# Optimization experiments

Measured on AMD Instinct MI355X. Metric: run time of the kernel, lower is better.

## Reference

```python
import jax, jax.numpy as jnp
import numpy as np

BITS = 4
MASK = (1 << BITS) - 1  # 15


def _dequant(qweight, scales, qzeros, groupsize):
    # qweight: [in//32*bits, out] int32; 8 nibbles packed per int32 along rows.
    out_f = qweight.shape[1]
    shifts = jnp.arange(0, 32, BITS, dtype=jnp.int32)  # [8]
    # [rows, 8, out] -> unpacked int weights in [0, 15]
    w = (qweight[:, None, :] >> shifts[None, :, None]) & MASK
    w = w.reshape(-1, groupsize, out_f)  # [n_groups, groupsize, out]
    s = scales.reshape(-1, 1, out_f)     # [n_groups, 1, out]
    z = qzeros.reshape(-1, 1, out_f)
    W = s * w.astype(scales.dtype) - z * s
    return W.reshape(-1, out_f)          # [in, out]


def setup_inputs() -> dict:
    key = jax.random.key(0)
    k1, k2, k3, k4, k5 = jax.random.split(key, 5)
    B, S, IN, OUT, G = 4, 2048, 4096, 4096, 64
    x = jax.random.normal(k1, (B, S, IN), dtype=jnp.float16)
    qweight = jax.random.randint(k2, (IN // 32 * BITS, OUT), 0, 2147483647, dtype=jnp.int32)
    scales = (jax.random.uniform(k3, (IN // G, OUT), dtype=jnp.float32) * 0.01 + 0.001).astype(jnp.float16)
    qzeros = (jax.random.uniform(k4, (IN // G, OUT), dtype=jnp.float32) * 15.0).astype(jnp.float16)
    bias = jax.random.normal(k5, (OUT,), dtype=jnp.float16)
    return {"x": x, "qweight": qweight, "scales": scales, "qzeros": qzeros,
            "bias": bias, "groupsize": G, "bits": BITS}


def reference(x, qweight, scales, qzeros, bias, groupsize, bits):
    W = _dequant(qweight, scales, qzeros, groupsize)  # [in, out] fp16
    return jnp.matmul(x, W) + bias
```

## Files before the change

kernel.cpp:

```cpp
#include <hip/hip_runtime.h>
#include <stdint.h>
#include <stddef.h>

typedef __bf16 bf16;
typedef __bf16 bf16x8 __attribute__((ext_vector_type(8)));
typedef float  f32x4  __attribute__((ext_vector_type(4)));

#define GLOBAL_AS(p) ((const __attribute__((address_space(1))) void*)(p))
#define LDS_AS(p)    ((__attribute__((address_space(3))) void*)(p))

__device__ __forceinline__ void gload_lds16(const bf16* g, bf16* l) {
    __builtin_amdgcn_global_load_lds(GLOBAL_AS(g), LDS_AS(l), 16, 0, 0);
}

__global__ __launch_bounds__(256)
void convert_x_kernel(const float* __restrict__ x, bf16* __restrict__ xb, long n8) {
    long t = (long)blockIdx.x * blockDim.x + threadIdx.x;
    if (t >= n8) return;
    const f32x4* p = (const f32x4*)(x + t * 8);
    f32x4 a = p[0], b = p[1];
    bf16x8 v;
#pragma unroll
    for (int j = 0; j < 4; ++j) { v[j] = (bf16)a[j]; v[4 + j] = (bf16)b[j]; }
    *(bf16x8*)(xb + t * 8) = v;
}

__global__ __launch_bounds__(256)
void dequant_wt64_kernel(const uint32_t* __restrict__ qw,
                         const float* __restrict__ scales,
                         const float* __restrict__ qzeros,
                         bf16* __restrict__ Wt,
                         int N, int K, int rows_per_group) {
    const int i = blockIdx.x * 256 + threadIdx.x;
    const int w = i >> 6, l = i & 63;
    const int nr8 = K >> 6;
    const int r8 = w % nr8;
    const int o  = (w / nr8) * 8 + (l >> 3);
    const int rr = l & 7;
    const int r  = r8 * 8 + rr;
    if (o >= N) return;
    const uint32_t q = qw[(size_t)r * N + o];
    const int g = r / rows_per_group;
    const float s = scales[(size_t)g * N + o];
    const float z = qzeros[(size_t)g * N + o];
    const float nsz = -s * z;
    bf16x8 v;
#pragma unroll
    for (int j = 0; j < 8; ++j)
        v[j] = (bf16)fmaf((float)((q >> (4 * j)) & 15u), s, nsz);
    *(bf16x8*)(Wt + ((size_t)r8 * N + o) * 64 + rr * 8) = v;
}

constexpr int BM2 = 256, BN2 = 256, BK2 = 64;

#define SB()    __builtin_amdgcn_sched_barrier(0)
#define BAR()   __builtin_amdgcn_s_barrier()
#define LGKM0() asm volatile("s_waitcnt lgkmcnt(0)" ::: "memory")
#define VMCNT(N) asm volatile("s_waitcnt vmcnt(" #N ")" ::: "memory")

#define MFMA_HALF(A, B, IBASE)                                             \
    _Pragma("unroll")                                                      \
    for (int i_ = 0; i_ < 4; ++i_) {                                       \
        _Pragma("unroll")                                                  \
        for (int j_ = 0; j_ < 4; ++j_)                                     \
            acc[(IBASE) + i_][j_] = __builtin_amdgcn_mfma_f32_16x16x32_bf16( \
                (A)[(IBASE) + i_], (B)[j_], acc[(IBASE) + i_][j_], 0, 0, 0); \
    }

#define PHASE_TAIL(A, B, IBASE)                          \
    SB();                                                \
    __builtin_amdgcn_s_setprio(1);                       \
    MFMA_HALF(A, B, IBASE);                              \
    __builtin_amdgcn_s_setprio(0);                       \
    LGKM0();                                             \
    BAR();                                               \
    SB()

#define PHASE_TAIL_VM4(A, B, IBASE)                      \
    SB();                                                \
    __builtin_amdgcn_s_setprio(1);                       \
    MFMA_HALF(A, B, IBASE);                              \
    __builtin_amdgcn_s_setprio(0);                       \
    LGKM0();                                             \
    VMCNT(4);                                            \
    BAR();                                               \
    SB()

#define READ_A4(DST, BUF, KH, LO)                                          \
    _Pragma("unroll")                                                      \
    for (int i_ = (LO); i_ < (LO) + 4; ++i_)                               \
        DST[i_] = *(const bf16x8*)(&As[BUF][(wm * 128 + i_ * 16 + lrow) * 64 \
                                           + (((lhi + 4 * (KH)) ^ swz) * 8)]);
#define READ_B4(DST, BUF, KH)                                              \
    _Pragma("unroll")                                                      \
    for (int j_ = 0; j_ < 4; ++j_)                                         \
        DST[j_] = *(const bf16x8*)(&Bs[BUF][(wn * 64 + j_ * 16 + lrow) * 64 \
                                           + (((lhi + 4 * (KH)) ^ swz) * 8)]);

__global__ __launch_bounds__(512, 2)
void gemm8_kernel(const bf16* __restrict__ Ab,
                  const bf16* __restrict__ Bt,
                  const float* __restrict__ bias,
                  float* __restrict__ out,
                  int M, int N, int K, int nbx) {
    __shared__ __align__(16) bf16 As[2][BM2 * BK2];
    __shared__ __align__(16) bf16 Bs[2][BN2 * BK2];

    const int tid  = threadIdx.x;
    const int lane = tid & 63;
    const int wave = tid >> 6;
    const int wm = wave >> 2;
    const int wn = wave & 3;

    const int nwg = gridDim.x;
    int wg = blockIdx.x;
    {
        const int q = nwg >> 3, r = nwg & 7;
        const int xcd = wg & 7, off = wg >> 3;
        wg = (xcd < r ? xcd * (q + 1) : r * (q + 1) + (xcd - r) * q) + off;
    }
    const int nby = nwg / nbx;
    const int bx = wg / nby;
    const int by = wg % nby;
    const int m0 = by * BM2;
    const int n0 = bx * BN2;

    const int lrow = lane & 15;
    const int lhi  = lane >> 4;
    const int swz  = (lrow >> 1) & 7;

    const int NT = K >> 6;
    const int NI = NT >> 1;

    const bf16* aSrc[2][2];
    const bf16* bSrc[2][2];
#pragma unroll
    for (int h = 0; h < 2; ++h)
#pragma unroll
        for (int it = 0; it < 2; ++it) {
            const int q  = tid + it * 512;
            const int rl = q >> 3;
            const int cl = (q & 7) ^ ((rl >> 1) & 7);
            aSrc[h][it] = Ab + (size_t)(m0 + h * 128 + rl) * K + cl * 8;
            bSrc[h][it] = Bt + (size_t)(n0 + h * 128 + rl) * 64 + cl * 8;
        }
    const size_t aStride = 64;
    const size_t bStride = (size_t)N * 64;

    auto stageA = [&](int tIdx, int buf) {
#pragma unroll
        for (int h = 0; h < 2; ++h)
#pragma unroll
            for (int it = 0; it < 2; ++it) {
                const int q = tid + it * 512;
                gload_lds16(aSrc[h][it] + (size_t)tIdx * aStride,
                            &As[buf][h * 8192 + q * 8]);
            }
    };
    auto stageB = [&](int tIdx, int buf) {
#pragma unroll
        for (int h = 0; h < 2; ++h)
#pragma unroll
            for (int it = 0; it < 2; ++it) {
                const int q = tid + it * 512;
                gload_lds16(bSrc[h][it] + (size_t)tIdx * bStride,
                            &Bs[buf][h * 8192 + q * 8]);
            }
    };

    f32x4 acc[8][4];
#pragma unroll
    for (int i = 0; i < 8; ++i)
#pragma unroll
        for (int j = 0; j < 4; ++j) acc[i][j] = (f32x4){0.f, 0.f, 0.f, 0.f};

    stageA(0, 0); stageB(0, 0); stageA(1, 1);
    VMCNT(4);
    BAR();
    SB();

    bf16x8 fa0[8], fa1[8], fb0[4], fb1[4];
    READ_A4(fa0, 0, 0, 0);
    READ_B4(fb0, 0, 0);

    for (int i2 = 0; i2 < NI; ++i2) {
        const int t0  = 2 * i2;
        const int tB1 = t0 + 1;
        const int tS2 = (t0 + 2 < NT) ? t0 + 2 : NT - 1;
        const int tS3 = (t0 + 3 < NT) ? t0 + 3 : NT - 1;

        READ_A4(fa0, 0, 0, 4);
        READ_B4(fb1, 0, 1);
        stageB(tB1, 1);
        PHASE_TAIL(fa0, fb0, 0);

        READ_A4(fa1, 0, 1, 0);
        PHASE_TAIL(fa0, fb0, 4);

        READ_A4(fa1, 0, 1, 4);
        stageB(tS2, 0);
        PHASE_TAIL_VM4(fa1, fb1, 0);

        READ_A4(fa0, 1, 0, 0);
        READ_B4(fb0, 1, 0);
        stageA(tS2, 0);
        PHASE_TAIL(fa1, fb1, 4);

        READ_A4(fa0, 1, 0, 4);
        READ_B4(fb1, 1, 1);
        PHASE_TAIL(fa0, fb0, 0);

        READ_A4(fa1, 1, 1, 0);
        READ_A4(fa1, 1, 1, 4);
        PHASE_TAIL(fa0, fb0, 4);

        stageA(tS3, 1);
        PHASE_TAIL_VM4(fa1, fb1, 0);

        READ_A4(fa0, 0, 0, 0);
        READ_B4(fb0, 0, 0);
        PHASE_TAIL(fa1, fb1, 4);
    }

    asm volatile("s_waitcnt vmcnt(0)" ::: "memory");

#pragma unroll
    for (int j = 0; j < 4; ++j) {
        const int col = n0 + wn * 64 + j * 16 + lrow;
        const float bv = bias[col];
#pragma unroll
        for (int i = 0; i < 8; ++i) {
            const int rbase = m0 + wm * 128 + i * 16 + lhi * 4;
#pragma unroll
            for (int r = 0; r < 4; ++r)
                out[(size_t)(rbase + r) * N + col] = acc[i][j][r] + bv;
        }
    }
}

constexpr int BM = 128, BN = 128, BK = 32;

__global__ __launch_bounds__(256)
void gemm_fused_kernel(const float* __restrict__ Af,
                       const uint32_t* __restrict__ qw,
                       const float* __restrict__ scales,
                       const float* __restrict__ qzeros,
                       const float* __restrict__ bias,
                       float* __restrict__ out,
                       int M, int N, int K, int G) {
    __shared__ __align__(16) bf16 As2[BM * BK];
    __shared__ __align__(16) bf16 Bs2[BN * BK];

    const int tid  = threadIdx.x;
    const int lane = tid & 63;
    const int wave = tid >> 6;
    const int wmm = wave & 1;
    const int wnn = wave >> 1;
    const int m0 = blockIdx.y * BM;
    const int n0 = blockIdx.x * BN;

    const int lr = lane & 15;
    const int lk8 = (lane >> 4) * 8;

    f32x4 acc[4][4];
#pragma unroll
    for (int i = 0; i < 4; ++i)
#pragma unroll
        for (int j = 0; j < 4; ++j) acc[i][j] = (f32x4){0.f, 0.f, 0.f, 0.f};

    for (int kt = 0; kt < K; kt += BK) {
#pragma unroll
        for (int it = 0; it < 2; ++it) {
            const int c = tid + it * 256;
            const int row = c >> 2;
            const int kc  = (c & 3) * 8;
            const f32x4* p = (const f32x4*)(Af + (size_t)(m0 + row) * K + kt + kc);
            f32x4 a = p[0], b = p[1];
            bf16x8 v;
#pragma unroll
            for (int j = 0; j < 4; ++j) { v[j] = (bf16)a[j]; v[4 + j] = (bf16)b[j]; }
            *(bf16x8*)(As2 + row * BK + kc) = v;
        }
        const int g = kt / G;
#pragma unroll
        for (int it = 0; it < 2; ++it) {
            const int idx = tid + it * 256;
            const int rl = idx >> 7;
            const int nl = idx & 127;
            uint32_t q = qw[(size_t)(kt / 8 + rl) * N + n0 + nl];
            float s = scales[(size_t)g * N + n0 + nl];
            float z = qzeros[(size_t)g * N + n0 + nl];
            float nsz = -s * z;
            bf16x8 v;
#pragma unroll
            for (int j = 0; j < 8; ++j)
                v[j] = (bf16)fmaf((float)((q >> (4 * j)) & 15u), s, nsz);
            *(bf16x8*)(Bs2 + nl * BK + rl * 8) = v;
        }
        __syncthreads();

        bf16x8 a[4], b[4];
#pragma unroll
        for (int i = 0; i < 4; ++i)
            a[i] = *(const bf16x8*)(As2 + (wmm * 64 + i * 16 + lr) * BK + lk8);
#pragma unroll
        for (int j = 0; j < 4; ++j)
            b[j] = *(const bf16x8*)(Bs2 + (wnn * 64 + j * 16 + lr) * BK + lk8);

#pragma unroll
        for (int i = 0; i < 4; ++i)
#pragma unroll
            for (int j = 0; j < 4; ++j)
                acc[i][j] = __builtin_amdgcn_mfma_f32_16x16x32_bf16(
                    a[i], b[j], acc[i][j], 0, 0, 0);
        __syncthreads();
    }

#pragma unroll
    for (int j = 0; j < 4; ++j) {
        const int col = n0 + wnn * 64 + j * 16 + (lane & 15);
        const float bv = bias[col];
#pragma unroll
        for (int i = 0; i < 4; ++i) {
            const int rbase = m0 + wmm * 64 + i * 16 + (lane >> 4) * 4;
#pragma unroll
            for (int r = 0; r < 4; ++r)
                out[(size_t)(rbase + r) * N + col] = acc[i][j][r] + bv;
        }
    }
}

extern "C" void kernel_launch(void* const* d_in, const int* in_sizes, int n_in,
                              void* d_out, int out_size, void* d_ws, size_t ws_size,
                              hipStream_t stream) {
    const float*    x      = (const float*)d_in[0];
    const uint32_t* qw     = (const uint32_t*)d_in[1];
    const float*    scales = (const float*)d_in[2];
    const float*    qzeros = (const float*)d_in[3];
    const float*    bias   = (const float*)d_in[4];
    float*          out    = (float*)d_out;

    const int N = in_sizes[4];
    const int K = (in_sizes[1] / N) * 8;
    const int M = in_sizes[0] / K;
    const int G = K / (in_sizes[2] / N);

    const size_t xb_bytes = (size_t)M * K * sizeof(bf16);
    const size_t wt_bytes = (size_t)N * K * sizeof(bf16);

    const bool shape_ok = (M % BM2 == 0) && (N % BN2 == 0) && (K % 128 == 0) &&
                          (G % 8 == 0);

    if (shape_ok && ws_size >= xb_bytes + wt_bytes) {
        bf16* Xb = (bf16*)d_ws;
        bf16* Wt = (bf16*)((char*)d_ws + xb_bytes);
        const long n8 = (long)M * K / 8;
        convert_x_kernel<<<(int)((n8 + 255) / 256), 256, 0, stream>>>(x, Xb, n8);
        const long dq_threads = ((long)K >> 6) * (N / 8) * 64;
        dequant_wt64_kernel<<<(int)((dq_threads + 255) / 256), 256, 0, stream>>>(
            qw, scales, qzeros, Wt, N, K, G / 8);
        const int nbx = N / BN2;
        const int nwg = nbx * (M / BM2);
        gemm8_kernel<<<nwg, 512, 0, stream>>>(Xb, Wt, bias, out, M, N, K, nbx);
    } else {
        dim3 grid(N / BN, M / BM);
        gemm_fused_kernel<<<grid, 256, 0, stream>>>(
            x, qw, scales, qzeros, bias, out, M, N, K, G);
    }
}
```

Measured before the change: 518.2 us.

## Restructure GEMM main loop with half-tile staging and relaxed LDS waits

Splits the A/B global-to-LDS staging into per-half loads interleaved across the eight MFMA phases, and reorders which operand is prefetched (B ahead by one tile instead of A). Most phases drop the full lgkmcnt(0) wait and barrier-per-phase in favor of partial lgkmcnt(8) waits and fewer waits, so LDS reads overlap more with MFMAs. This aims to spread memory traffic evenly and cut stall time at barriers, but risks race hazards if the looser waits let reads see buffers still being overwritten.

```diff
diff --git a/kernel.cpp b/kernel.cpp
--- a/kernel.cpp
+++ b/kernel.cpp
@@ -55,8 +55,10 @@
 
 #define SB()    __builtin_amdgcn_sched_barrier(0)
 #define BAR()   __builtin_amdgcn_s_barrier()
-#define LGKM0() asm volatile("s_waitcnt lgkmcnt(0)" ::: "memory")
+#define LGKM(N) asm volatile("s_waitcnt lgkmcnt(" #N ")" ::: "memory")
 #define VMCNT(N) asm volatile("s_waitcnt vmcnt(" #N ")" ::: "memory")
+#define PRIO1() __builtin_amdgcn_s_setprio(1)
+#define PRIO0() __builtin_amdgcn_s_setprio(0)
 
 #define MFMA_HALF(A, B, IBASE)                                             \
     _Pragma("unroll")                                                      \
@@ -66,25 +68,6 @@
             acc[(IBASE) + i_][j_] = __builtin_amdgcn_mfma_f32_16x16x32_bf16( \
                 (A)[(IBASE) + i_], (B)[j_], acc[(IBASE) + i_][j_], 0, 0, 0); \
     }
-
-#define PHASE_TAIL(A, B, IBASE)                          \
-    SB();                                                \
-    __builtin_amdgcn_s_setprio(1);                       \
-    MFMA_HALF(A, B, IBASE);                              \
-    __builtin_amdgcn_s_setprio(0);                       \
-    LGKM0();                                             \
-    BAR();                                               \
-    SB()
-
-#define PHASE_TAIL_VM4(A, B, IBASE)                      \
-    SB();                                                \
-    __builtin_amdgcn_s_setprio(1);                       \
-    MFMA_HALF(A, B, IBASE);                              \
-    __builtin_amdgcn_s_setprio(0);                       \
-    LGKM0();                                             \
-    VMCNT(4);                                            \
-    BAR();                                               \
-    SB()
 
 #define READ_A4(DST, BUF, KH, LO)                                          \
     _Pragma("unroll")                                                      \
@@ -147,25 +130,21 @@
     const size_t aStride = 64;
     const size_t bStride = (size_t)N * 64;
 
-    auto stageA = [&](int tIdx, int buf) {
-#pragma unroll
-        for (int h = 0; h < 2; ++h)
-#pragma unroll
-            for (int it = 0; it < 2; ++it) {
-                const int q = tid + it * 512;
-                gload_lds16(aSrc[h][it] + (size_t)tIdx * aStride,
-                            &As[buf][h * 8192 + q * 8]);
-            }
+    auto stageAh = [&](int tIdx, int half, int buf) {
+#pragma unroll
+        for (int it = 0; it < 2; ++it) {
+            const int q = tid + it * 512;
+            gload_lds16(aSrc[half][it] + (size_t)tIdx * aStride,
+                        &As[buf][half * 8192 + q * 8]);
+        }
     };
-    auto stageB = [&](int tIdx, int buf) {
-#pragma unroll
-        for (int h = 0; h < 2; ++h)
-#pragma unroll
-            for (int it = 0; it < 2; ++it) {
-                const int q = tid + it * 512;
-                gload_lds16(bSrc[h][it] + (size_t)tIdx * bStride,
-                            &Bs[buf][h * 8192 + q * 8]);
-            }
+    auto stageBh = [&](int tIdx, int half, int buf) {
+#pragma unroll
+        for (int it = 0; it < 2; ++it) {
+            const int q = tid + it * 512;
+            gload_lds16(bSrc[half][it] + (size_t)tIdx * bStride,
+                        &Bs[buf][half * 8192 + q * 8]);
+        }
     };
 
     f32x4 acc[8][4];
@@ -174,52 +153,79 @@
 #pragma unroll
         for (int j = 0; j < 4; ++j) acc[i][j] = (f32x4){0.f, 0.f, 0.f, 0.f};
 
-    stageA(0, 0); stageB(0, 0); stageA(1, 1);
+    stageAh(0, 0, 0); stageAh(0, 1, 0); stageBh(0, 0, 0); stageBh(0, 1, 0);
+    stageBh(1, 0, 1); stageBh(1, 1, 1);
     VMCNT(4);
     BAR();
     SB();
 
     bf16x8 fa0[8], fa1[8], fb0[4], fb1[4];
-    READ_A4(fa0, 0, 0, 0);
-    READ_B4(fb0, 0, 0);
 
     for (int i2 = 0; i2 < NI; ++i2) {
-        const int t0  = 2 * i2;
-        const int tB1 = t0 + 1;
-        const int tS2 = (t0 + 2 < NT) ? t0 + 2 : NT - 1;
-        const int tS3 = (t0 + 3 < NT) ? t0 + 3 : NT - 1;
-
+        const int tE  = 2 * i2;
+        const int tO  = tE + 1;
+        const int tE2 = (tE + 2 < NT) ? tE + 2 : NT - 1;
+        const int tO2 = (tE + 3 < NT) ? tE + 3 : NT - 1;
+
+        READ_A4(fa0, 0, 0, 0);
+        READ_B4(fb0, 0, 0);
         READ_A4(fa0, 0, 0, 4);
+        stageAh(tO, 0, 1);
+        SB();
+        PRIO1(); MFMA_HALF(fa0, fb0, 0); PRIO0();
+        BAR(); SB();
+
         READ_B4(fb1, 0, 1);
-        stageB(tB1, 1);
-        PHASE_TAIL(fa0, fb0, 0);
-
+        SB();
         READ_A4(fa1, 0, 1, 0);
-        PHASE_TAIL(fa0, fb0, 4);
-
         READ_A4(fa1, 0, 1, 4);
-        stageB(tS2, 0);
-        PHASE_TAIL_VM4(fa1, fb1, 0);
+        stageAh(tO, 1, 1);
+        SB();
+        PRIO1(); MFMA_HALF(fa0, fb0, 4); PRIO0();
+        LGKM(8); SB();
+        BAR(); SB();
+
+        stageBh(tE2, 0, 0);
+        SB();
+        PRIO1(); MFMA_HALF(fa1, fb1, 0); PRIO0();
+        BAR(); SB();
+
+        stageBh(tE2, 1, 0);
+        SB();
+        PRIO1(); MFMA_HALF(fa1, fb1, 4); PRIO0();
+        LGKM(0); SB();
+        VMCNT(4);
+        BAR(); SB();
 
         READ_A4(fa0, 1, 0, 0);
         READ_B4(fb0, 1, 0);
-        stageA(tS2, 0);
-        PHASE_TAIL(fa1, fb1, 4);
-
         READ_A4(fa0, 1, 0, 4);
+        stageAh(tE2, 0, 0);
+        SB();
+        PRIO1(); MFMA_HALF(fa0, fb0, 0); PRIO0();
+        BAR(); SB();
+
         READ_B4(fb1, 1, 1);
-        PHASE_TAIL(fa0, fb0, 0);
-
+        SB();
         READ_A4(fa1, 1, 1, 0);
         READ_A4(fa1, 1, 1, 4);
-        PHASE_TAIL(fa0, fb0, 4);
-
-        stageA(tS3, 1);
-        PHASE_TAIL_VM4(fa1, fb1, 0);
-
-        READ_A4(fa0, 0, 0, 0);
-        READ_B4(fb0, 0, 0);
-        PHASE_TAIL(fa1, fb1, 4);
+        stageAh(tE2, 1, 0);
+        SB();
+        PRIO1(); MFMA_HALF(fa0, fb0, 4); PRIO0();
+        LGKM(8); SB();
+        BAR(); SB();
+
+        stageBh(tO2, 0, 1);
+        SB();
+        PRIO1(); MFMA_HALF(fa1, fb1, 0); PRIO0();
+        BAR(); SB();
+
+        stageBh(tO2, 1, 1);
+        SB();
+        PRIO1(); MFMA_HALF(fa1, fb1, 4); PRIO0();
+        LGKM(0); SB();
+        VMCNT(4);
+        BAR(); SB();
     }
 
     asm volatile("s_waitcnt vmcnt(0)" ::: "memory");
```

Measured after the change: 478.7 us. 1.08x faster.
